# Kernel optimization log

Hardware: AMD Instinct MI355X
Metric: run time of the kernel (lower is better)

Reference implementation:

```python
import jax, jax.numpy as jnp
import numpy as np

# DAttentionBaseline config (matches init_kwargs)
NH, HC, G = 8, 32, 4          # n_heads, n_head_channels, n_groups
ORF = 2.0                      # offset_range_factor
KK = 5                         # offset conv kernel (stage_idx=2)


def _conv1x1(x, w, b=None):
    # x: (B,C,H,W), w: (O,C)
    y = jnp.einsum('bchw,oc->bohw', x, w)
    return y if b is None else y + b[None, :, None, None]


def _ref_points(Hk, Wk, dtype):
    # replicates torch.meshgrid(..., indexing='xy') as in the source
    ly = jnp.linspace(0.5, Hk - 0.5, Hk, dtype=dtype)
    lx = jnp.linspace(0.5, Wk - 0.5, Wk, dtype=dtype)
    ry, rx = jnp.meshgrid(ly, lx, indexing='xy')  # shapes (Wk, Hk); Hk==Wk here
    return jnp.stack([ry / Hk * 2 - 1, rx / Wk * 2 - 1], axis=-1)  # (Hk,Wk,2)


def _grid_sample(img, grid):
    # bilinear, align_corners=True, zero padding. img:(N,C,Hi,Wi), grid:(N,Hg,Wg,2) in [-1,1] (x,y)
    N, C, Hi, Wi = img.shape
    gx = (grid[..., 0] + 1.0) * 0.5 * (Wi - 1)
    gy = (grid[..., 1] + 1.0) * 0.5 * (Hi - 1)
    x0 = jnp.floor(gx); y0 = jnp.floor(gy)
    x1 = x0 + 1.0;      y1 = y0 + 1.0
    wx1 = gx - x0; wx0 = 1.0 - wx1
    wy1 = gy - y0; wy0 = 1.0 - wy1
    nidx = jnp.arange(N)[:, None, None]

    def gather(yf, xf):
        valid = (xf >= 0) & (xf <= Wi - 1) & (yf >= 0) & (yf <= Hi - 1)
        xi = jnp.clip(xf, 0, Wi - 1).astype(jnp.int32)
        yi = jnp.clip(yf, 0, Hi - 1).astype(jnp.int32)
        vals = img[nidx, :, yi, xi]  # (N,Hg,Wg,C)
        return vals * valid[..., None].astype(img.dtype)

    out = (gather(y0, x0) * (wy0 * wx0)[..., None]
           + gather(y0, x1) * (wy0 * wx1)[..., None]
           + gather(y1, x0) * (wy1 * wx0)[..., None]
           + gather(y1, x1) * (wy1 * wx1)[..., None])
    return out.transpose(0, 3, 1, 2)  # (N,C,Hg,Wg)


def _forward(x, wq, bq, w_off_dw, b_off_dw, ln_g, ln_b, w_off_pj, wk, bk, wv, bv, wo, bo, rpe_table):
    B, C, H, W = x.shape
    GC = C // G            # group channels
    GH = NH // G           # group heads
    scale = HC ** -0.5

    q = _conv1x1(x, wq, bq)                                   # (B,C,H,W)
    q_off = q.reshape(B * G, GC, H, W)

    # conv_offset: depthwise conv -> LayerNorm over channels -> GELU -> 1x1 conv to 2
    off = jax.lax.conv_general_dilated(
        q_off, w_off_dw, (1, 1), [(KK // 2, KK // 2), (KK // 2, KK // 2)],
        feature_group_count=GC, dimension_numbers=('NCHW', 'OIHW', 'NCHW'))
    off = off + b_off_dw[None, :, None, None]
    mu = off.mean(axis=1, keepdims=True)
    var = off.var(axis=1, keepdims=True)
    off = (off - mu) * jax.lax.rsqrt(var + 1e-5)
    off = off * ln_g[None, :, None, None] + ln_b[None, :, None, None]
    off = jax.nn.gelu(off, approximate=False)
    offset = jnp.einsum('bchw,oc->bohw', off, w_off_pj)       # (B*G,2,Hk,Wk)

    Hk, Wk = offset.shape[2], offset.shape[3]
    ns = Hk * Wk
    rng = jnp.array([1.0 / Hk, 1.0 / Wk], dtype=x.dtype).reshape(1, 2, 1, 1)
    offset = jnp.tanh(offset) * rng * ORF                     # offset_range_factor > 0
    offset = offset.transpose(0, 2, 3, 1)                     # (B*G,Hk,Wk,2)

    ref = _ref_points(Hk, Wk, x.dtype)                        # (Hk,Wk,2)
    pos = offset + ref[None]                                  # (B*G,Hk,Wk,2), (y,x) order

    xs = _grid_sample(x.reshape(B * G, GC, H, W), pos[..., ::-1])  # (B*G,GC,Hk,Wk)
    xs = xs.reshape(B, C, 1, ns)

    k = _conv1x1(xs, wk, bk).reshape(B * NH, HC, ns)
    v = _conv1x1(xs, wv, bv).reshape(B * NH, HC, ns)
    qf = q.reshape(B * NH, HC, H * W)
    attn = jnp.einsum('bcm,bcn->bmn', qf, k) * scale          # (B*NH, HW, ns)

    # RPE via grid_sample on the (2H-1, 2W-1) bias table
    rpe = jnp.broadcast_to(rpe_table[None], (B,) + rpe_table.shape)
    rpe = rpe.reshape(B * G, GH, 2 * H - 1, 2 * W - 1)
    qg = _ref_points(H, W, x.dtype).reshape(H * W, 2)
    disp = (qg[None, :, None, :] - pos.reshape(B * G, ns, 2)[:, None, :, :]) * 0.5  # (B*G,HW,ns,2)
    bias = _grid_sample(rpe, disp[..., ::-1]).reshape(B * NH, H * W, ns)
    attn = attn + bias

    attn = jax.nn.softmax(attn, axis=2)
    out = jnp.einsum('bmn,bcn->bcm', attn, v).reshape(B, C, H, W)
    y = _conv1x1(out, wo, bo)
    return (y,
            pos.reshape(B, G, Hk, Wk, 2),
            jnp.broadcast_to(ref[None, None], (B, G, Hk, Wk, 2)))


def setup_inputs() -> dict:
    key = jax.random.key(0)
    ks = jax.random.split(key, 8)
    B, C, H, W = 4, 256, 32, 32
    GC = C // G
    s = 0.02

    def n(k, shape, sc=s):
        return jax.random.normal(k, shape, jnp.float32) * sc

    return {
        'x': jax.random.normal(ks[0], (B, C, H, W), jnp.float32),
        'wq': n(ks[1], (C, C)), 'bq': jnp.zeros((C,), jnp.float32),
        'w_off_dw': n(ks[2], (GC, 1, KK, KK)), 'b_off_dw': jnp.zeros((GC,), jnp.float32),
        'ln_g': jnp.ones((GC,), jnp.float32), 'ln_b': jnp.zeros((GC,), jnp.float32),
        'w_off_pj': n(ks[3], (2, GC)),
        'wk': n(ks[4], (C, C)), 'bk': jnp.zeros((C,), jnp.float32),
        'wv': n(ks[5], (C, C)), 'bv': jnp.zeros((C,), jnp.float32),
        'wo': n(ks[6], (C, C)), 'bo': jnp.zeros((C,), jnp.float32),
        'rpe_table': n(ks[7], (NH, 2 * H - 1, 2 * W - 1), 0.01),
    }


def reference(x, wq, bq, w_off_dw, b_off_dw, ln_g, ln_b, w_off_pj, wk, bk, wv, bv, wo, bo, rpe_table):
    return _forward(x, wq, bq, w_off_dw, b_off_dw, ln_g, ln_b, w_off_pj, wk, bk, wv, bv, wo, bo, rpe_table)
```

## Files before the change

### kernel.cpp

```cpp
#include <hip/hip_runtime.h>
#include <math.h>

#define CK __restrict__

constexpr int CH = 256;
constexpr int HW = 1024;

typedef __attribute__((ext_vector_type(8))) short short8;
typedef __attribute__((ext_vector_type(4))) float f32x4;
typedef __attribute__((ext_vector_type(2))) float v2f;

__device__ __forceinline__ ushort f2b(float x) {
    union { float f; unsigned int u; } a; a.f = x;
    unsigned int r = (a.u + 0x7FFFu + ((a.u >> 16) & 1u)) >> 16;
    return (ushort)r;
}
__device__ __forceinline__ short8 ld8(const ushort* p) { return *(const short8*)p; }
__device__ __forceinline__ float u2f(unsigned int u) {
    union { unsigned int u; float f; } a; a.u = u; return a.f;
}
__device__ __forceinline__ float b2f(ushort us) { return u2f((unsigned int)us << 16); }

__global__ __launch_bounds__(256) void prep(const float* CK w0, const float* CK w1,
                                            const float* CK w2, const float* CK w3,
                                            ushort* CK o0, ushort* CK o1,
                                            ushort* CK o2, ushort* CK o3,
                                            const float* CK x, ushort* CK xT,
                                            const float* CK rpe, unsigned int* CK rpetab) {
    const int bid = blockIdx.x, t = threadIdx.x;
    if (bid < 256) {
        const float* src; ushort* dst;
        switch (bid >> 6) {
            case 0: src = w0; dst = o0; break;
            case 1: src = w1; dst = o1; break;
            case 2: src = w2; dst = o2; break;
            default: src = w3; dst = o3; break;
        }
        const int i = (bid & 63) * 256 + t;
        float4 v = ((const float4*)src)[i];
        ushort4 r; r.x = f2b(v.x); r.y = f2b(v.y); r.z = f2b(v.z); r.w = f2b(v.w);
        ((ushort4*)dst)[i] = r;
    } else if (bid < 384) {
        const int b2 = bid - 256;
        const int c8 = b2 & 31, b = b2 >> 5;
        for (int nn = 0; nn < 4; nn++) {
            const int n = nn * 256 + t;
            union { ushort u[8]; short8 s; } pk;
#pragma unroll
            for (int j = 0; j < 8; j++) pk.u[j] = f2b(x[(b * 256 + c8 * 8 + j) * HW + n]);
            *(short8*)(xT + b * 262144 + n * 256 + c8 * 8) = pk.s;
        }
    } else {
        const int h = bid - 384;
        const float* rp = rpe + h * 3969;
        unsigned int* dst = rpetab + h * 4356;
        for (int i = t; i < 4356; i += 256) {
            int y = i / 67, x2 = i - y * 67;
            int yy = y - 1, xx = x2 - 1;
            bool vy = (yy >= 0) && (yy < 63) && (y < 65);
            float a  = (vy && xx >= 0 && xx < 63) ? rp[yy * 63 + xx] : 0.f;
            float bb = (vy && xx >= -1 && xx < 62) ? rp[yy * 63 + xx + 1] : 0.f;
            dst[i] = (unsigned int)f2b(a) | ((unsigned int)f2b(bb) << 16);
        }
    }
}

__global__ __launch_bounds__(256) void gemm_q(const ushort* CK AT, const ushort* CK W,
                                              const float* CK bias, ushort* CK Y) {
    const int b = blockIdx.z;
    const int t = threadIdx.x, w = t >> 6, l = t & 63;
    const int lm = l & 15, qd = l >> 4;
    const int m0 = blockIdx.y * 64 + (w & 1) * 32;
    const int n0 = blockIdx.x * 64 + (w >> 1) * 32;
    const ushort* A = AT + b * 262144 + n0 * 256;
    const ushort* Bm = W + m0 * 256;
    f32x4 acc[2][2] = {};
#pragma unroll
    for (int k0 = 0; k0 < 8; k0++) {
        const int ko = k0 * 32 + qd * 8;
        short8 a0 = ld8(A + lm * 256 + ko);
        short8 a1 = ld8(A + (16 + lm) * 256 + ko);
        short8 b0 = ld8(Bm + lm * 256 + ko);
        short8 b1 = ld8(Bm + (16 + lm) * 256 + ko);
        acc[0][0] = __builtin_amdgcn_mfma_f32_16x16x32_bf16(a0, b0, acc[0][0], 0, 0, 0);
        acc[0][1] = __builtin_amdgcn_mfma_f32_16x16x32_bf16(a0, b1, acc[0][1], 0, 0, 0);
        acc[1][0] = __builtin_amdgcn_mfma_f32_16x16x32_bf16(a1, b0, acc[1][0], 0, 0, 0);
        acc[1][1] = __builtin_amdgcn_mfma_f32_16x16x32_bf16(a1, b1, acc[1][1], 0, 0, 0);
    }
#pragma unroll
    for (int in = 0; in < 2; in++)
#pragma unroll
        for (int im = 0; im < 2; im++) {
            const int m = m0 + im * 16 + lm;
            const float bs = bias[m];
            ushort4 r;
            r.x = f2b(acc[in][im][0] + bs); r.y = f2b(acc[in][im][1] + bs);
            r.z = f2b(acc[in][im][2] + bs); r.w = f2b(acc[in][im][3] + bs);
            *(ushort4*)(Y + b * 262144 + m * HW + n0 + in * 16 + qd * 4) = r;
        }
}

__global__ __launch_bounds__(256) void gemm_kv(const ushort* CK AT,
                                               const ushort* CK Wk, const float* CK bk, ushort* CK kbt,
                                               const ushort* CK Wv, const float* CK bv, ushort* CK vbs) {
    const int b = blockIdx.z;
    const int t = threadIdx.x, w = t >> 6, l = t & 63;
    const int lm = l & 15, qd = l >> 4;
    const int m0 = blockIdx.y * 64 + (w & 1) * 32;
    const int n0 = blockIdx.x * 64 + (w >> 1) * 32;
    const ushort* A = AT + b * 262144 + n0 * 256;
    const ushort* Bk = Wk + m0 * 256;
    const ushort* Bv = Wv + m0 * 256;
    f32x4 akT[2][2] = {}, av[2][2] = {};
#pragma unroll
    for (int k0 = 0; k0 < 8; k0++) {
        const int ko = k0 * 32 + qd * 8;
        short8 a0 = ld8(A + lm * 256 + ko);
        short8 a1 = ld8(A + (16 + lm) * 256 + ko);
        short8 k0f = ld8(Bk + lm * 256 + ko);
        short8 k1f = ld8(Bk + (16 + lm) * 256 + ko);
        short8 v0f = ld8(Bv + lm * 256 + ko);
        short8 v1f = ld8(Bv + (16 + lm) * 256 + ko);
        akT[0][0] = __builtin_amdgcn_mfma_f32_16x16x32_bf16(k0f, a0, akT[0][0], 0, 0, 0);
        akT[0][1] = __builtin_amdgcn_mfma_f32_16x16x32_bf16(k0f, a1, akT[0][1], 0, 0, 0);
        akT[1][0] = __builtin_amdgcn_mfma_f32_16x16x32_bf16(k1f, a0, akT[1][0], 0, 0, 0);
        akT[1][1] = __builtin_amdgcn_mfma_f32_16x16x32_bf16(k1f, a1, akT[1][1], 0, 0, 0);
        av[0][0] = __builtin_amdgcn_mfma_f32_16x16x32_bf16(a0, v0f, av[0][0], 0, 0, 0);
        av[0][1] = __builtin_amdgcn_mfma_f32_16x16x32_bf16(a0, v1f, av[0][1], 0, 0, 0);
        av[1][0] = __builtin_amdgcn_mfma_f32_16x16x32_bf16(a1, v0f, av[1][0], 0, 0, 0);
        av[1][1] = __builtin_amdgcn_mfma_f32_16x16x32_bf16(a1, v1f, av[1][1], 0, 0, 0);
    }
#pragma unroll
    for (int im = 0; im < 2; im++)
#pragma unroll
        for (int in = 0; in < 2; in++) {
            {
                const int c0 = m0 + im * 16 + qd * 4;
                const int n  = n0 + in * 16 + lm;
                const int bh = b * 8 + (c0 >> 5);
                const int qdk = (c0 & 31) >> 3, co4 = c0 & 7;
                const int nc = n >> 7, nbk = (n >> 4) & 7, lmk = n & 15;
                const float4 bks = *(const float4*)(bk + c0);
                ushort4 r4;
                r4.x = f2b(akT[im][in][0] + bks.x);
                r4.y = f2b(akT[im][in][1] + bks.y);
                r4.z = f2b(akT[im][in][2] + bks.z);
                r4.w = f2b(akT[im][in][3] + bks.w);
                *(ushort4*)(kbt + ((bh * 8 + nc) * 512 + nbk * 64 + qdk * 16 + lmk) * 8 + co4) = r4;
            }
            {
                const int c = m0 + im * 16 + lm;
                const int bh = b * 8 + (c >> 5);
                const float bs = bv[c];
                const int cb = (c & 31) >> 4, lmv = c & 15;
                const int nbase = n0 + in * 16 + qd * 4;
                const int nc = nbase >> 7, kc = (nbase >> 5) & 3;
                const int qdv = (nbase >> 3) & 3, co0 = nbase & 7;
                ushort4 r4;
                r4.x = f2b(av[in][im][0] + bs); r4.y = f2b(av[in][im][1] + bs);
                r4.z = f2b(av[in][im][2] + bs); r4.w = f2b(av[in][im][3] + bs);
                *(ushort4*)(vbs + ((bh * 8 + nc) * 512 + (cb * 4 + kc) * 64 + qdv * 16 + lmv) * 8 + co0) = r4;
            }
        }
}

__global__ __launch_bounds__(256) void dwconv(const ushort* CK q, const float* CK wdw,
                                              const float* CK bdw, float* CK off) {
    const int bx = blockIdx.x;
    const int ch = bx & 63;
    const ushort* qb = q + bx * HW;
    float w[25];
#pragma unroll
    for (int i = 0; i < 25; i++) w[i] = wdw[ch * 25 + i];
    const float bb = bdw[ch];
    const int t = threadIdx.x;
#pragma unroll
    for (int p = 0; p < 4; p++) {
        int hw = p * 256 + t;
        int ii = hw >> 5, jj = hw & 31;
        float s = bb;
#pragma unroll
        for (int ky = 0; ky < 5; ky++) {
            int y = ii + ky - 2;
            if (y < 0 || y > 31) continue;
#pragma unroll
            for (int kx = 0; kx < 5; kx++) {
                int x = jj + kx - 2;
                if (x < 0 || x > 31) continue;
                s += b2f(qb[y * 32 + x]) * w[ky * 5 + kx];
            }
        }
        off[bx * HW + hw] = s;
    }
}

__global__ __launch_bounds__(256) void lnps(const float* CK off, const float* CK ln_g,
                                            const float* CK ln_b, const float* CK wpj,
                                            const float* CK x,
                                            float* CK out_pos, float* CK out_ref,
                                            float2* CK pos_sc, ushort* CK xsT) {
    const int bid = blockIdx.x, t = threadIdx.x;
    const int bg = bid >> 4;
    const int pix_l = t >> 2, qtr = t & 3;
    const int n = (bid & 15) * 64 + pix_l;
    const int gid = bg * 1024 + n;
    const float* ob = off + bg * 64 * HW + n;
    const int c0 = qtr * 16;
    float v[16];
    float s1 = 0.f;
#pragma unroll
    for (int j = 0; j < 16; j++) { v[j] = ob[(c0 + j) * HW]; s1 += v[j]; }
    s1 += __shfl_xor(s1, 1); s1 += __shfl_xor(s1, 2);
    const float mean = s1 * 0.015625f;
    float s2 = 0.f;
#pragma unroll
    for (int j = 0; j < 16; j++) { float d = v[j] - mean; s2 += d * d; }
    s2 += __shfl_xor(s2, 1); s2 += __shfl_xor(s2, 2);
    const float rs = rsqrtf(s2 * 0.015625f + 1e-5f);
    float p0 = 0.f, p1 = 0.f;
#pragma unroll
    for (int j = 0; j < 16; j++) {
        float vv = (v[j] - mean) * rs * ln_g[c0 + j] + ln_b[c0 + j];
        float gl = 0.5f * vv * (1.f + erff(vv * 0.70710678118654752f));
        p0 += gl * wpj[c0 + j];
        p1 += gl * wpj[64 + c0 + j];
    }
    p0 += __shfl_xor(p0, 1); p0 += __shfl_xor(p0, 2);
    p1 += __shfl_xor(p1, 1); p1 += __shfl_xor(p1, 2);
    const int ii = n >> 5, jj = n & 31;
    const float r0 = (jj + 0.5f) * 0.0625f - 1.f;
    const float r1 = (ii + 0.5f) * 0.0625f - 1.f;
    const float pos0 = tanhf(p0) * 0.0625f + r0;
    const float pos1 = tanhf(p1) * 0.0625f + r1;
    if (qtr == 0) {
        out_pos[gid * 2] = pos0; out_pos[gid * 2 + 1] = pos1;
        out_ref[gid * 2] = r0;   out_ref[gid * 2 + 1] = r1;
        pos_sc[gid].x = pos0 * 15.5f; pos_sc[gid].y = pos1 * 15.5f;
    }
    const float gx = (pos1 + 1.f) * 15.5f, gy = (pos0 + 1.f) * 15.5f;
    const float x0f = floorf(gx), y0f = floorf(gy);
    const float wx1 = gx - x0f, wx0 = 1.f - wx1, wy1 = gy - y0f, wy0 = 1.f - wy1;
    const bool vx0 = (x0f >= 0.f) && (x0f <= 31.f);
    const bool vx1 = (x0f >= -1.f) && (x0f <= 30.f);
    const bool vy0 = (y0f >= 0.f) && (y0f <= 31.f);
    const bool vy1 = (y0f >= -1.f) && (y0f <= 30.f);
    const int xi0 = (int)fminf(fmaxf(x0f, 0.f), 31.f);
    const int xi1 = (int)fminf(fmaxf(x0f + 1.f, 0.f), 31.f);
    const int yi0 = (int)fminf(fmaxf(y0f, 0.f), 31.f);
    const int yi1 = (int)fminf(fmaxf(y0f + 1.f, 0.f), 31.f);
    const float w00 = (vy0 && vx0) ? wy0 * wx0 : 0.f;
    const float w01 = (vy0 && vx1) ? wy0 * wx1 : 0.f;
    const float w10 = (vy1 && vx0) ? wy1 * wx0 : 0.f;
    const float w11 = (vy1 && vx1) ? wy1 * wx1 : 0.f;
    const int o00 = yi0 * 32 + xi0, o01 = yi0 * 32 + xi1;
    const int o10 = yi1 * 32 + xi0, o11 = yi1 * 32 + xi1;
    const int b = bg >> 2, g = bg & 3;
    const float* xb = x + bg * 64 * HW;
    ushort* xo = xsT + b * 262144 + n * 256 + g * 64 + c0;
#pragma unroll
    for (int j4 = 0; j4 < 4; j4++) {
        ushort4 r4;
        float vals[4];
#pragma unroll
        for (int j = 0; j < 4; j++) {
            const float* p = xb + (c0 + j4 * 4 + j) * HW;
            vals[j] = w00 * p[o00] + w01 * p[o01] + w10 * p[o10] + w11 * p[o11];
        }
        r4.x = f2b(vals[0]); r4.y = f2b(vals[1]); r4.z = f2b(vals[2]); r4.w = f2b(vals[3]);
        *(ushort4*)(xo + j4 * 4) = r4;
    }
}

__global__ __launch_bounds__(256, 4) void attn_part(const ushort* CK q, const ushort* CK kbt,
                                                    const ushort* CK vbs, const float2* CK pos_sc,
                                                    const unsigned int* CK rpetab,
                                                    ushort* CK partO, float* CK lbuf) {
    __shared__ __align__(16) unsigned int rpe_pr[4356];
    __shared__ __align__(16) ushort Pl[4][1088];
    const int bh = blockIdx.y, quarter = blockIdx.z;
    const int b = bh >> 3, nh = bh & 7, bg = bh >> 1;
    const int t = threadIdx.x;
    const int w = t >> 6, l = t & 63;
    const int lm = l & 15, qd = l >> 4;

    {
        const uint4* src4 = (const uint4*)(rpetab + nh * 4356);
        uint4* dst4 = (uint4*)rpe_pr;
        for (int i = t; i < 1089; i += 256) dst4[i] = src4[i];
    }
    __syncthreads();

    const int m = blockIdx.x * 64 + w * 16 + lm;
    short8 qf;
    {
        union { ushort u[8]; short8 s; } pk;
        const ushort* qb = q + (b * 256 + nh * 32) * HW + m;
#pragma unroll
        for (int j = 0; j < 8; j++) pk.u[j] = qb[(qd * 8 + j) * HW];
        qf = pk.s;
    }
    const float qg0 = ((m & 31) + 0.5f) * 0.0625f - 1.f;
    const float qg1 = ((m >> 5) + 0.5f) * 0.0625f - 1.f;
    const float ax = 31.f + 15.5f * qg1;
    const float ay = 31.f + 15.5f * qg0;

    f32x4 oacc0 = {0.f, 0.f, 0.f, 0.f}, oacc1 = {0.f, 0.f, 0.f, 0.f};
    float rsum = 0.f;
    ushort* PlW = Pl[w];
    const float2* pbase = pos_sc + bg * 1024;

    for (int nc = quarter * 2; nc < quarter * 2 + 2; nc++) {
        const ushort* kg = kbt + (bh * 8 + nc) * 4096;
        const ushort* vg = vbs + (bh * 8 + nc) * 4096;

#pragma unroll
        for (int g = 0; g < 2; g++) {
            f32x4 sT[4];
#pragma unroll
            for (int s = 0; s < 4; s++) {
                const int nb = g * 4 + s;
                sT[s] = __builtin_amdgcn_mfma_f32_16x16x32_bf16(
                            ld8(kg + (nb * 64 + l) * 8), qf,
                            (f32x4){0.f, 0.f, 0.f, 0.f}, 0, 0, 0);
            }
#pragma unroll
            for (int s = 0; s < 4; s++) {
                const float4* pp = (const float4*)(pbase + nc * 128 + (g * 4 + s) * 16 + qd * 4);
                const float4 pa = pp[0], pb_ = pp[1];
                const float psx[4] = {pa.x, pa.z, pb_.x, pb_.z};
                const float psy[4] = {pa.y, pa.w, pb_.y, pb_.w};
#pragma unroll
                for (int rp = 0; rp < 2; rp++) {
                    v2f gx = {ax - psy[rp * 2], ax - psy[rp * 2 + 1]};
                    v2f gy = {ay - psx[rp * 2], ay - psx[rp * 2 + 1]};
                    const int xi0 = (int)gx.x, xi1 = (int)gx.y;
                    const int yi0 = (int)gy.x, yi1 = (int)gy.y;
                    v2f wx = gx - (v2f){(float)xi0, (float)xi1};
                    v2f wy = gy - (v2f){(float)yi0, (float)yi1};
                    const int idxA = yi0 * 67 + xi0 + 68;
                    const int idxB = yi1 * 67 + xi1 + 68;
                    const unsigned int a0 = rpe_pr[idxA], a1 = rpe_pr[idxA + 67];
                    const unsigned int b0 = rpe_pr[idxB], b1 = rpe_pr[idxB + 67];
                    v2f tA = {u2f(a0 << 16), u2f(a0 & 0xFFFF0000u)};
                    v2f bA = {u2f(a1 << 16), u2f(a1 & 0xFFFF0000u)};
                    v2f tB = {u2f(b0 << 16), u2f(b0 & 0xFFFF0000u)};
                    v2f bB = {u2f(b1 << 16), u2f(b1 & 0xFFFF0000u)};
                    v2f vA = tA + wy.x * (bA - tA);
                    v2f vB = tB + wy.y * (bB - tB);
                    const float biasA = vA.x + wx.x * (vA.y - vA.x);
                    const float biasB = vB.x + wx.y * (vB.y - vB.x);
                    sT[s][rp * 2]     = sT[s][rp * 2]     * 0.17677669529663687f + biasA;
                    sT[s][rp * 2 + 1] = sT[s][rp * 2 + 1] * 0.17677669529663687f + biasB;
                }
            }
#pragma unroll
            for (int s = 0; s < 4; s++) {
                float e0 = __expf(sT[s][0]);
                float e1 = __expf(sT[s][1]);
                float e2 = __expf(sT[s][2]);
                float e3 = __expf(sT[s][3]);
                rsum += (e0 + e1) + (e2 + e3);
                uint2 pk;
                pk.x = (unsigned int)f2b(e0) | ((unsigned int)f2b(e1) << 16);
                pk.y = (unsigned int)f2b(e2) | ((unsigned int)f2b(e3) << 16);
                *(uint2*)(PlW + s * 272 + l * 4) = pk;
            }
#pragma unroll
            for (int kc = 0; kc < 2; kc++) {
                const ushort* pb2 = PlW + (kc * 2 + (qd >> 1)) * 272 + (qd & 1) * 128 + lm * 4;
                union { uint2 u[2]; short8 s; } pfu;
                pfu.u[0] = *(const uint2*)pb2;
                pfu.u[1] = *(const uint2*)(pb2 + 64);
                const int kv = g * 2 + kc;
                oacc0 = __builtin_amdgcn_mfma_f32_16x16x32_bf16(ld8(vg + (kv * 64 + l) * 8), pfu.s, oacc0, 0, 0, 0);
                oacc1 = __builtin_amdgcn_mfma_f32_16x16x32_bf16(ld8(vg + ((4 + kv) * 64 + l) * 8), pfu.s, oacc1, 0, 0, 0);
            }
        }
    }

    rsum += __shfl_xor(rsum, 16);
    rsum += __shfl_xor(rsum, 32);

    ushort* po = partO + (((quarter * 32 + bh) * 1024 + m) * 32) + qd * 4;
    ushort4 r04, r14;
    r04.x = f2b(oacc0[0]); r04.y = f2b(oacc0[1]); r04.z = f2b(oacc0[2]); r04.w = f2b(oacc0[3]);
    r14.x = f2b(oacc1[0]); r14.y = f2b(oacc1[1]); r14.z = f2b(oacc1[2]); r14.w = f2b(oacc1[3]);
    *(ushort4*)po = r04;
    *(ushort4*)(po + 16) = r14;
    if (qd == 0) lbuf[(quarter * 32 + bh) * 1024 + m] = rsum;
}

__global__ __launch_bounds__(256) void gemm_oc(const ushort* CK partO, const float* CK lbuf,
                                               const ushort* CK W, const float* CK bias,
                                               float* CK Y) {
    __shared__ __align__(16) float ew[64][8];
    const int b = blockIdx.z;
    const int t = threadIdx.x, w = t >> 6, l = t & 63;
    const int lm = l & 15, qd = l >> 4;
    const int m0 = blockIdx.y * 64 + (w & 1) * 32;
    const int n0 = blockIdx.x * 64 + (w >> 1) * 32;
    const int nblk = blockIdx.x * 64;

    for (int p = t; p < 512; p += 256) {
        const int pix = p >> 3, head = p & 7;
        const int mg = nblk + pix;
        const int bh = b * 8 + head;
        float den = 0.f;
#pragma unroll
        for (int q2 = 0; q2 < 4; q2++) den += lbuf[(q2 * 32 + bh) * 1024 + mg];
        ew[pix][head] = 1.f / den;
    }
    __syncthreads();

    const ushort* Bm = W + m0 * 256;
    f32x4 acc[2][2] = {};
#pragma unroll
    for (int k0 = 0; k0 < 8; k0++) {
        const int ko = k0 * 32 + qd * 8;
        short8 af[2];
#pragma unroll
        for (int half = 0; half < 2; half++) {
            const int pix_l = (w >> 1) * 32 + half * 16 + lm;
            const int mg = nblk + pix_l;
            const ushort* pbq = partO + ((b * 8 + k0) * 1024 + mg) * 32 + qd * 8;
            const float inv = ew[pix_l][k0];
            float a8[8] = {};
#pragma unroll
            for (int q2 = 0; q2 < 4; q2++) {
                union { ushort u[8]; short8 s; } pv;
                pv.s = ld8(pbq + q2 * 1048576);
#pragma unroll
                for (int j = 0; j < 8; j++) a8[j] += b2f(pv.u[j]);
            }
            union { ushort u[8]; short8 s; } out;
#pragma unroll
            for (int j = 0; j < 8; j++) out.u[j] = f2b(a8[j] * inv);
            af[half] = out.s;
        }
        short8 b0 = ld8(Bm + lm * 256 + ko);
        short8 b1 = ld8(Bm + (16 + lm) * 256 + ko);
        acc[0][0] = __builtin_amdgcn_mfma_f32_16x16x32_bf16(af[0], b0, acc[0][0], 0, 0, 0);
        acc[0][1] = __builtin_amdgcn_mfma_f32_16x16x32_bf16(af[0], b1, acc[0][1], 0, 0, 0);
        acc[1][0] = __builtin_amdgcn_mfma_f32_16x16x32_bf16(af[1], b0, acc[1][0], 0, 0, 0);
        acc[1][1] = __builtin_amdgcn_mfma_f32_16x16x32_bf16(af[1], b1, acc[1][1], 0, 0, 0);
    }
#pragma unroll
    for (int in = 0; in < 2; in++)
#pragma unroll
        for (int im = 0; im < 2; im++) {
            const int mo = m0 + im * 16 + lm;
            const float bs = bias[mo];
            float4 r;
            r.x = acc[in][im][0] + bs; r.y = acc[in][im][1] + bs;
            r.z = acc[in][im][2] + bs; r.w = acc[in][im][3] + bs;
            *(float4*)(Y + b * 262144 + mo * HW + n0 + in * 16 + qd * 4) = r;
        }
}

extern "C" void kernel_launch(void* const* d_in, const int* in_sizes, int n_in,
                              void* d_out, int out_size, void* d_ws, size_t ws_size,
                              hipStream_t stream) {
    (void)in_sizes; (void)n_in; (void)out_size; (void)ws_size;
    const float* x   = (const float*)d_in[0];
    const float* wq  = (const float*)d_in[1];
    const float* bq  = (const float*)d_in[2];
    const float* wdw = (const float*)d_in[3];
    const float* bdw = (const float*)d_in[4];
    const float* lng = (const float*)d_in[5];
    const float* lnb = (const float*)d_in[6];
    const float* wpj = (const float*)d_in[7];
    const float* wk  = (const float*)d_in[8];
    const float* bk  = (const float*)d_in[9];
    const float* wv  = (const float*)d_in[10];
    const float* bv  = (const float*)d_in[11];
    const float* wo  = (const float*)d_in[12];
    const float* bo  = (const float*)d_in[13];
    const float* rpe = (const float*)d_in[14];
    float* outp = (float*)d_out;
    char* base = (char*)d_ws;
    const size_t MB = 1 << 20;

    ushort* q_b    = (ushort*)(base);
    ushort* kbt    = (ushort*)(base + 2 * MB);
    ushort* vbs    = (ushort*)(base + 4 * MB);
    float*  off_ws = (float*)(base + 6 * MB);
    ushort* xT     = (ushort*)(base + 10 * MB);
    ushort* xsT    = (ushort*)(base + 12 * MB);
    ushort* partO  = (ushort*)(base + 6 * MB);
    float*  lbuf   = (float*)(base + 14 * MB);
    ushort* wqb    = (ushort*)(base + 15 * MB);
    ushort* wkb    = (ushort*)(base + 15 * MB + 131072);
    ushort* wvb    = (ushort*)(base + 15 * MB + 262144);
    ushort* wob    = (ushort*)(base + 15 * MB + 393216);
    float2* pos_sc = (float2*)(base + 15 * MB + 524288);
    unsigned int* rpetab = (unsigned int*)(base + 15 * MB + 655360);

    prep<<<392, 256, 0, stream>>>(wq, wk, wv, wo, wqb, wkb, wvb, wob, x, xT, rpe, rpetab);
    gemm_q<<<dim3(16, 4, 4), 256, 0, stream>>>(xT, wqb, bq, q_b);
    dwconv<<<1024, 256, 0, stream>>>(q_b, wdw, bdw, off_ws);
    lnps<<<256, 256, 0, stream>>>(off_ws, lng, lnb, wpj, x,
                                  outp + (1 << 20), outp + (1 << 20) + 32768, pos_sc, xsT);
    gemm_kv<<<dim3(16, 4, 4), 256, 0, stream>>>(xsT, wkb, bk, kbt, wvb, bv, vbs);
    attn_part<<<dim3(16, 32, 4), 256, 0, stream>>>(q_b, kbt, vbs, pos_sc, rpetab, partO, lbuf);
    gemm_oc<<<dim3(16, 4, 4), 256, 0, stream>>>(partO, lbuf, wob, bo, outp);
}
```

Measured before the change: 183.5 us.

## Fuse depthwise offset conv into LayerNorm/projection kernel via shared-memory tiles

Merges the separate depthwise 5x5 conv kernel into the LayerNorm+GELU+projection kernel. Each block stages a halo'd tile of 6 rows by 64 channels of bf16 q into LDS, computes the conv from register sliding windows, and writes results to an LDS tile that the LN stage reads directly. This removes one launch and the 4 MB fp32 offset round trip through global memory. In exchange the fused kernel uses more LDS and registers, and the conv now runs on 256 blocks instead of 1024.

```diff
diff --git a/kernel.cpp b/kernel.cpp
--- a/kernel.cpp
+++ b/kernel.cpp
@@ -164,52 +164,86 @@
         }
 }
 
-__global__ __launch_bounds__(256) void dwconv(const ushort* CK q, const float* CK wdw,
-                                              const float* CK bdw, float* CK off) {
-    const int bx = blockIdx.x;
-    const int ch = bx & 63;
-    const ushort* qb = q + bx * HW;
-    float w[25];
-#pragma unroll
-    for (int i = 0; i < 25; i++) w[i] = wdw[ch * 25 + i];
-    const float bb = bdw[ch];
-    const int t = threadIdx.x;
-#pragma unroll
-    for (int p = 0; p < 4; p++) {
-        int hw = p * 256 + t;
-        int ii = hw >> 5, jj = hw & 31;
-        float s = bb;
-#pragma unroll
-        for (int ky = 0; ky < 5; ky++) {
-            int y = ii + ky - 2;
-            if (y < 0 || y > 31) continue;
-#pragma unroll
-            for (int kx = 0; kx < 5; kx++) {
-                int x = jj + kx - 2;
-                if (x < 0 || x > 31) continue;
-                s += b2f(qb[y * 32 + x]) * w[ky * 5 + kx];
-            }
-        }
-        off[bx * HW + hw] = s;
-    }
-}
-
-__global__ __launch_bounds__(256) void lnps(const float* CK off, const float* CK ln_g,
+__global__ __launch_bounds__(256) void dwln(const ushort* CK q, const float* CK wdw,
+                                            const float* CK bdw, const float* CK ln_g,
                                             const float* CK ln_b, const float* CK wpj,
                                             const float* CK x,
                                             float* CK out_pos, float* CK out_ref,
                                             float2* CK pos_sc, ushort* CK xsT) {
+    __shared__ __align__(16) ushort qs[64 * 218];
+    __shared__ __align__(16) float offs[64][68];
     const int bid = blockIdx.x, t = threadIdx.x;
-    const int bg = bid >> 4;
+    const int bg = bid >> 4, rp = bid & 15;
+
+    {
+        const int ch = t & 63;
+        const int r6a = t >> 6;
+#pragma unroll
+        for (int pass = 0; pass < 2; pass++) {
+            const int r6 = (pass == 0) ? r6a : (4 + r6a);
+            if (pass == 1 && r6a >= 2) break;
+            const int grow = rp * 2 - 2 + r6;
+            unsigned int* dst = (unsigned int*)(qs + ch * 218 + r6 * 36);
+            if (grow >= 0 && grow <= 31) {
+                const unsigned int* src = (const unsigned int*)(q + (bg * 64 + ch) * 1024 + grow * 32);
+                dst[0] = 0;
+#pragma unroll
+                for (int k2 = 0; k2 < 16; k2++) dst[1 + k2] = src[k2];
+                dst[17] = 0;
+            } else {
+#pragma unroll
+                for (int k2 = 0; k2 < 18; k2++) dst[k2] = 0;
+            }
+        }
+    }
+    __syncthreads();
+
+    {
+        const int ch = t >> 2, pg = t & 3;
+        const int pr = pg >> 1, c0 = (pg & 1) * 16;
+        float w[25];
+#pragma unroll
+        for (int i = 0; i < 25; i++) w[i] = wdw[ch * 25 + i];
+        const float bb = bdw[ch];
+        float nb[5][20];
+#pragma unroll
+        for (int r = 0; r < 5; r++) {
+            const unsigned int* row = (const unsigned int*)(qs + ch * 218 + (pr + r) * 36 + c0);
+#pragma unroll
+            for (int u = 0; u < 10; u++) {
+                const unsigned int v = row[u];
+                nb[r][u * 2]     = u2f(v << 16);
+                nb[r][u * 2 + 1] = u2f(v & 0xFFFF0000u);
+            }
+        }
+#pragma unroll
+        for (int j = 0; j < 16; j++) {
+            float s = bb;
+#pragma unroll
+            for (int ky = 0; ky < 5; ky++)
+#pragma unroll
+                for (int kx = 0; kx < 5; kx++) s += nb[ky][j + kx] * w[ky * 5 + kx];
+            offs[pr * 32 + c0 + j][ch] = s;
+        }
+    }
+    __syncthreads();
+
     const int pix_l = t >> 2, qtr = t & 3;
-    const int n = (bid & 15) * 64 + pix_l;
+    const int n = rp * 64 + pix_l;
     const int gid = bg * 1024 + n;
-    const float* ob = off + bg * 64 * HW + n;
     const int c0 = qtr * 16;
     float v[16];
+    {
+        const float4* ov = (const float4*)&offs[pix_l][c0];
+        const float4 V0 = ov[0], V1 = ov[1], V2 = ov[2], V3 = ov[3];
+        v[0] = V0.x;  v[1] = V0.y;  v[2] = V0.z;  v[3] = V0.w;
+        v[4] = V1.x;  v[5] = V1.y;  v[6] = V1.z;  v[7] = V1.w;
+        v[8] = V2.x;  v[9] = V2.y;  v[10] = V2.z; v[11] = V2.w;
+        v[12] = V3.x; v[13] = V3.y; v[14] = V3.z; v[15] = V3.w;
+    }
     float s1 = 0.f;
 #pragma unroll
-    for (int j = 0; j < 16; j++) { v[j] = ob[(c0 + j) * HW]; s1 += v[j]; }
+    for (int j = 0; j < 16; j++) s1 += v[j];
     s1 += __shfl_xor(s1, 1); s1 += __shfl_xor(s1, 2);
     const float mean = s1 * 0.015625f;
     float s2 = 0.f;
@@ -483,7 +517,6 @@
     ushort* q_b    = (ushort*)(base);
     ushort* kbt    = (ushort*)(base + 2 * MB);
     ushort* vbs    = (ushort*)(base + 4 * MB);
-    float*  off_ws = (float*)(base + 6 * MB);
     ushort* xT     = (ushort*)(base + 10 * MB);
     ushort* xsT    = (ushort*)(base + 12 * MB);
     ushort* partO  = (ushort*)(base + 6 * MB);
@@ -497,8 +530,7 @@
 
     prep<<<392, 256, 0, stream>>>(wq, wk, wv, wo, wqb, wkb, wvb, wob, x, xT, rpe, rpetab);
     gemm_q<<<dim3(16, 4, 4), 256, 0, stream>>>(xT, wqb, bq, q_b);
-    dwconv<<<1024, 256, 0, stream>>>(q_b, wdw, bdw, off_ws);
-    lnps<<<256, 256, 0, stream>>>(off_ws, lng, lnb, wpj, x,
+    dwln<<<256, 256, 0, stream>>>(q_b, wdw, bdw, lng, lnb, wpj, x,
                                   outp + (1 << 20), outp + (1 << 20) + 32768, pos_sc, xsT);
     gemm_kv<<<dim3(16, 4, 4), 256, 0, stream>>>(xsT, wkb, bk, kbt, wvb, bv, vbs);
     attn_part<<<dim3(16, 32, 4), 256, 0, stream>>>(q_b, kbt, vbs, pos_sc, rpetab, partO, lbuf);
```

New measurement: 168.3 us. 8.3% less time.
